# Kernel optimization log

Hardware: AMD Instinct MI355X
Metric: run time of the kernel (lower is better)

## Reference

```python
import jax, jax.numpy as jnp
import numpy as np

B, N, C, CP, H, NK = 1, 2048, 128, 16, 8, 128
D = C // H
W_HALF = NK // 2
EPS = 1e-5
NEG = -1e9


def _ln(x, scale=None, bias=None):
    m = jnp.mean(x, axis=-1, keepdims=True)
    v = jnp.var(x, axis=-1, keepdims=True)
    y = (x - m) * jax.lax.rsqrt(v + EPS)
    if scale is not None:
        y = y * scale
    if bias is not None:
        y = y + bias
    return y


def _ada_ln(a, s, s_scale, gate_w, gate_b, skip_w):
    # AF3 AdaLN: a <- sigmoid(Lin(LN(s))) * LN(a) + LinNoBias(LN(s))
    sn = _ln(s, s_scale)
    return jax.nn.sigmoid(sn @ gate_w + gate_b) * _ln(a) + sn @ skip_w


def setup_inputs() -> dict:
    key = jax.random.key(0)
    ks = jax.random.split(key, 24)

    def w(k, shape, fan_in):
        return jax.random.normal(k, shape, jnp.float32) / np.float32(np.sqrt(fan_in))

    return {
        'atom_single_repr': jax.random.normal(ks[0], (B, N, C), jnp.float32),
        'atom_single_proj': jax.random.normal(ks[1], (B, N, C), jnp.float32),
        'atom_pair_repr': jax.random.normal(ks[2], (B, N, N, CP), jnp.float32),
        'mask': jnp.ones((B, N), jnp.float32),
        # AttentionPairBias AdaLN
        'adaln_s_scale': jnp.ones((C,), jnp.float32),
        'adaln_gate_w': w(ks[3], (C, C), C),
        'adaln_gate_b': jnp.zeros((C,), jnp.float32),
        'adaln_skip_w': w(ks[4], (C, C), C),
        # attention projections
        'wq': w(ks[5], (C, H * D), C),
        'wk': w(ks[6], (C, H * D), C),
        'wv': w(ks[7], (C, H * D), C),
        'wg': w(ks[8], (C, H * D), C),
        'bg': jnp.ones((H * D,), jnp.float32),
        'wo': w(ks[9], (H * D, C), H * D),
        'bo': jnp.zeros((C,), jnp.float32),
        # pair bias
        'pair_ln_scale': jnp.ones((CP,), jnp.float32),
        'pair_ln_bias': jnp.zeros((CP,), jnp.float32),
        'w_pair': w(ks[10], (CP, H), CP),
        # adaLN-zero output gate (bias init -2)
        'out_gate_w': w(ks[11], (C, C), C),
        'out_gate_b': jnp.full((C,), -2.0, jnp.float32),
        # ConditionedTransitionBlock AdaLN
        't_s_scale': jnp.ones((C,), jnp.float32),
        't_gate_w': w(ks[12], (C, C), C),
        't_gate_b': jnp.zeros((C,), jnp.float32),
        't_skip_w': w(ks[13], (C, C), C),
        # SwiGLU transition, expansion n=2
        't_swish_w': w(ks[14], (C, 2 * C), C),
        't_hidden_w': w(ks[15], (C, 2 * C), C),
        't_out_w': w(ks[16], (2 * C, C), 2 * C),
        't_out_gate_w': w(ks[17], (C, C), C),
        't_out_gate_b': jnp.full((C,), -2.0, jnp.float32),
    }


def reference(atom_single_repr, atom_single_proj, atom_pair_repr, mask,
              adaln_s_scale, adaln_gate_w, adaln_gate_b, adaln_skip_w,
              wq, wk, wv, wg, bg, wo, bo,
              pair_ln_scale, pair_ln_bias, w_pair,
              out_gate_w, out_gate_b,
              t_s_scale, t_gate_w, t_gate_b, t_skip_w,
              t_swish_w, t_hidden_w, t_out_w, t_out_gate_w, t_out_gate_b):
    b, n, _ = atom_single_repr.shape
    # --- AttentionPairBias ---
    a = _ada_ln(atom_single_repr, atom_single_proj,
                adaln_s_scale, adaln_gate_w, adaln_gate_b, adaln_skip_w)
    # pair bias [b,h,n,n]
    bias = jnp.transpose(_ln(atom_pair_repr, pair_ln_scale, pair_ln_bias) @ w_pair, (0, 3, 1, 2))
    idx = jnp.arange(n)
    diff = idx[None, :] - idx[:, None]  # j - i
    win = (diff >= -W_HALF) & (diff <= W_HALF)  # sliding window (left,right)=(64,64)
    bias = bias + jnp.where(win, 0.0, NEG)[None, None]
    bias = bias + (1e9 * (mask - 1.0))[:, None, None, :]
    q = (a @ wq).reshape(b, n, H, D) * (D ** -0.5)
    k = (a @ wk).reshape(b, n, H, D)
    v = (a @ wv).reshape(b, n, H, D)
    attn = jax.nn.softmax(jnp.einsum('bqhd,bkhd->bhqk', q, k) + bias, axis=-1)
    o = jnp.einsum('bhqk,bkhd->bqhd', attn, v)
    g = jax.nn.sigmoid(a @ wg + bg).reshape(b, n, H, D)  # per-head output gating
    attn_out = (o * g).reshape(b, n, H * D) @ wo + bo
    attn_out = jax.nn.sigmoid(atom_single_proj @ out_gate_w + out_gate_b) * attn_out
    # --- ConditionedTransitionBlock ---
    t = _ada_ln(atom_single_repr, atom_single_proj,
                t_s_scale, t_gate_w, t_gate_b, t_skip_w)
    hid = jax.nn.silu(t @ t_swish_w) * (t @ t_hidden_w)  # SwiGLU
    trans = jax.nn.sigmoid(atom_single_proj @ t_out_gate_w + t_out_gate_b) * (hid @ t_out_w)
    return attn_out + trans
```

## Files before the change

### kernel.cpp

```cpp
#include <hip/hip_runtime.h>

#define NN 2048
#define CC 128
#define CPC 16
#define HH 8
#define DD 16
#define WHALF 64

__device__ __forceinline__ float sigf(float x){ return 1.0f/(1.0f+__expf(-x)); }

__global__ __launch_bounds__(256) void ln_both(const float* __restrict__ a,
                                               const float* __restrict__ s,
                                               float* __restrict__ ln_a,
                                               float* __restrict__ ln_s){
  const float* x = blockIdx.y ? s : a;
  float* ln = blockIdx.y ? ln_s : ln_a;
  int row = blockIdx.x*4 + (threadIdx.x>>6);
  int lane = threadIdx.x & 63;
  size_t base = (size_t)row*CC;
  float2 v = *(const float2*)(x + base + 2*lane);
  float ssum = v.x+v.y, sq = v.x*v.x+v.y*v.y;
  #pragma unroll
  for (int m=32;m;m>>=1){ ssum += __shfl_xor(ssum,m); sq += __shfl_xor(sq,m); }
  float mean = ssum*(1.0f/CC);
  float var  = sq*(1.0f/CC)-mean*mean;
  float inv  = rsqrtf(var+1e-5f);
  float2 o; o.x=(v.x-mean)*inv; o.y=(v.y-mean)*inv;
  *(float2*)(ln + base + 2*lane) = o;
}

template<int K, int RPT, int NM>
__device__ __forceinline__ void gemm_core(const float* __restrict__ Arows,
                                          const float* __restrict__ scale,
                                          const float* __restrict__ W0,
                                          const float* __restrict__ W1,
                                          int ldw, int colBase,
                                          float acc[NM][RPT][4], float* As){
  const int t = threadIdx.x;
  constexpr int ROWS = RPT*8;
  const int nv = ROWS*K/4;
  for (int i=t;i<nv;i+=256){
    float4 v = ((const float4*)Arows)[i];
    if (scale){
      int kk = (i*4)&(K-1);
      v.x*=scale[kk]; v.y*=scale[kk+1]; v.z*=scale[kk+2]; v.w*=scale[kk+3];
    }
    ((float4*)As)[i]=v;
  }
  __syncthreads();
  const int tr = t>>5;
  const int col = colBase + (t&31)*4;
  #pragma unroll
  for(int m=0;m<NM;m++)
    #pragma unroll
    for(int r=0;r<RPT;r++){ acc[m][r][0]=0;acc[m][r][1]=0;acc[m][r][2]=0;acc[m][r][3]=0; }
  #pragma unroll 4
  for (int k=0;k<K;k++){
    float a[RPT];
    #pragma unroll
    for (int r=0;r<RPT;r++) a[r]=As[(tr*RPT+r)*K+k];
    {
      float4 w = *(const float4*)(W0 + (size_t)k*ldw + col);
      #pragma unroll
      for (int r=0;r<RPT;r++){acc[0][r][0]+=a[r]*w.x;acc[0][r][1]+=a[r]*w.y;acc[0][r][2]+=a[r]*w.z;acc[0][r][3]+=a[r]*w.w;}
    }
    if constexpr (NM>1){
      float4 w = *(const float4*)(W1 + (size_t)k*ldw + col);
      #pragma unroll
      for (int r=0;r<RPT;r++){acc[1][r][0]+=a[r]*w.x;acc[1][r][1]+=a[r]*w.y;acc[1][r][2]+=a[r]*w.z;acc[1][r][3]+=a[r]*w.w;}
    }
  }
}

__global__ __launch_bounds__(256) void k_gates(const float* __restrict__ s,
    const float* __restrict__ W0, const float* __restrict__ b0,
    const float* __restrict__ W1, const float* __restrict__ b1,
    float* __restrict__ sgog, float* __restrict__ sgtg){
  __shared__ float As[8*128];
  float acc[2][1][4];
  const int row0 = blockIdx.x*8;
  gemm_core<128,1,2>(s + (size_t)row0*CC, nullptr, W0, W1, 128, 0, acc, As);
  const int col = (threadIdx.x&31)*4;
  const int row = row0 + (threadIdx.x>>5);
  float4 v0 = *(const float4*)(b0+col);
  float4 v1 = *(const float4*)(b1+col);
  float4 o0, o1;
  o0.x=sigf(acc[0][0][0]+v0.x); o0.y=sigf(acc[0][0][1]+v0.y); o0.z=sigf(acc[0][0][2]+v0.z); o0.w=sigf(acc[0][0][3]+v0.w);
  o1.x=sigf(acc[1][0][0]+v1.x); o1.y=sigf(acc[1][0][1]+v1.y); o1.z=sigf(acc[1][0][2]+v1.z); o1.w=sigf(acc[1][0][3]+v1.w);
  *(float4*)(sgog + (size_t)row*CC + col) = o0;
  *(float4*)(sgtg + (size_t)row*CC + col) = o1;
}

__global__ __launch_bounds__(256) void k_adaln(const float* __restrict__ ln_s,
    const float* __restrict__ sscale,
    const float* __restrict__ gate_w, const float* __restrict__ gate_b,
    const float* __restrict__ skip_w, const float* __restrict__ ln_a,
    float* __restrict__ outp){
  __shared__ float As[8*128];
  float acc[2][1][4];
  const int row0 = blockIdx.x*8;
  gemm_core<128,1,2>(ln_s + (size_t)row0*CC, sscale, gate_w, skip_w, 128, 0, acc, As);
  const int col = (threadIdx.x&31)*4;
  const int row = row0 + (threadIdx.x>>5);
  float4 gb = *(const float4*)(gate_b+col);
  float4 la = *(const float4*)(ln_a + (size_t)row*CC + col);
  float4 o;
  o.x = sigf(acc[0][0][0]+gb.x)*la.x + acc[1][0][0];
  o.y = sigf(acc[0][0][1]+gb.y)*la.y + acc[1][0][1];
  o.z = sigf(acc[0][0][2]+gb.z)*la.z + acc[1][0][2];
  o.w = sigf(acc[0][0][3]+gb.w)*la.w + acc[1][0][3];
  *(float4*)(outp + (size_t)row*CC + col) = o;
}

__global__ __launch_bounds__(256) void k_qkvg(const float* __restrict__ A,
    const float* __restrict__ wq, const float* __restrict__ wk,
    const float* __restrict__ wv, const float* __restrict__ wg,
    const float* __restrict__ bg,
    float* __restrict__ qb, float* __restrict__ kb,
    float* __restrict__ vb, float* __restrict__ gg){
  __shared__ float As[16*128];
  float acc[2][2][4];
  const int row0 = blockIdx.x*16;
  const int y = blockIdx.y;
  const float* W0 = y ? wv : wq;
  const float* W1 = y ? wg : wk;
  gemm_core<128,2,2>(A + (size_t)row0*CC, nullptr, W0, W1, 128, 0, acc, As);
  const int col = (threadIdx.x&31)*4;
  float* O0 = y ? vb : qb;
  float* O1 = y ? gg : kb;
  float4 b1 = {0,0,0,0};
  if (y) b1 = *(const float4*)(bg+col);
  #pragma unroll
  for (int r=0;r<2;r++){
    const int row = row0 + (threadIdx.x>>5)*2 + r;
    float4 o0 = {acc[0][r][0],acc[0][r][1],acc[0][r][2],acc[0][r][3]};
    float4 o1 = {acc[1][r][0]+b1.x,acc[1][r][1]+b1.y,acc[1][r][2]+b1.z,acc[1][r][3]+b1.w};
    *(float4*)(O0 + (size_t)row*CC + col) = o0;
    *(float4*)(O1 + (size_t)row*CC + col) = o1;
  }
}

__global__ __launch_bounds__(256) void k_wo(const float* __restrict__ A,
    const float* __restrict__ W, const float* __restrict__ b,
    float* __restrict__ outp){
  __shared__ float As[8*128];
  float acc[1][1][4];
  const int row0 = blockIdx.x*8;
  gemm_core<128,1,1>(A + (size_t)row0*CC, nullptr, W, nullptr, 128, 0, acc, As);
  const int col = (threadIdx.x&31)*4;
  const int row = row0 + (threadIdx.x>>5);
  float4 bb = *(const float4*)(b+col);
  float4 o = {acc[0][0][0]+bb.x, acc[0][0][1]+bb.y, acc[0][0][2]+bb.z, acc[0][0][3]+bb.w};
  *(float4*)(outp + (size_t)row*CC + col) = o;
}

__global__ __launch_bounds__(256) void k_swiglu(const float* __restrict__ A,
    const float* __restrict__ sw_w, const float* __restrict__ hd_w,
    float* __restrict__ hid){
  __shared__ float As[8*128];
  float acc[2][1][4];
  const int row0 = blockIdx.x*8;
  const int cb = blockIdx.y*128;
  gemm_core<128,1,2>(A + (size_t)row0*CC, nullptr, sw_w, hd_w, 256, cb, acc, As);
  const int col = cb + (threadIdx.x&31)*4;
  const int row = row0 + (threadIdx.x>>5);
  float4 o;
  o.x = acc[0][0][0]*sigf(acc[0][0][0])*acc[1][0][0];
  o.y = acc[0][0][1]*sigf(acc[0][0][1])*acc[1][0][1];
  o.z = acc[0][0][2]*sigf(acc[0][0][2])*acc[1][0][2];
  o.w = acc[0][0][3]*sigf(acc[0][0][3])*acc[1][0][3];
  *(float4*)(hid + (size_t)row*256 + col) = o;
}

__global__ __launch_bounds__(256) void k_tout(const float* __restrict__ hid,
    const float* __restrict__ W,
    const float* __restrict__ sgog, const float* __restrict__ aout,
    const float* __restrict__ sgtg, float* __restrict__ outp){
  __shared__ float As[8*256];
  float acc[1][1][4];
  const int row0 = blockIdx.x*8;
  gemm_core<256,1,1>(hid + (size_t)row0*256, nullptr, W, nullptr, 128, 0, acc, As);
  const int col = (threadIdx.x&31)*4;
  const int row = row0 + (threadIdx.x>>5);
  float4 g0 = *(const float4*)(sgog + (size_t)row*CC + col);
  float4 ao = *(const float4*)(aout + (size_t)row*CC + col);
  float4 g1 = *(const float4*)(sgtg + (size_t)row*CC + col);
  float4 o;
  o.x = g0.x*ao.x + g1.x*acc[0][0][0];
  o.y = g0.y*ao.y + g1.y*acc[0][0][1];
  o.z = g0.z*ao.z + g1.z*acc[0][0][2];
  o.w = g0.w*ao.w + g1.w*acc[0][0][3];
  *(float4*)(outp + (size_t)row*CC + col) = o;
}

__global__ __launch_bounds__(256) void attn_win(const float* __restrict__ q,
    const float* __restrict__ k, const float* __restrict__ v,
    const float* __restrict__ g, const float* __restrict__ pair,
    const float* __restrict__ pls, const float* __restrict__ plb,
    const float* __restrict__ w_pair, const float* __restrict__ mask,
    float* __restrict__ o_out) {
  __shared__ __align__(16) float qs[CC];
  __shared__ float sc[HH][132];
  __shared__ float wp[CPC][HH];
  __shared__ float plss[CPC], plbs[CPC];
  __shared__ float inv_sum[HH];
  const int i = blockIdx.x;
  const int t = threadIdx.x;
  if (t < CC) qs[t] = q[(size_t)i*CC + t] * 0.25f;
  if (t < CPC*HH) wp[t>>3][t&7] = w_pair[t];
  if (t >= 128 && t < 128+CPC){ plss[t-128]=pls[t-128]; plbs[t-128]=plb[t-128]; }
  __syncthreads();
  const int jlo = (i-WHALF > 0) ? i-WHALF : 0;
  const int jhi = (i+WHALF < NN-1) ? i+WHALF : NN-1;
  const int nj = jhi - jlo + 1;
  if (t < nj){
    const int j = jlo + t;
    float pv[CPC]; float s=0.f, sq=0.f;
    const float4* pp4 = (const float4*)(pair + ((size_t)i*NN + j)*CPC);
    #pragma unroll
    for (int c4=0;c4<CPC/4;c4++){
      float4 x4 = pp4[c4];
      pv[c4*4]=x4.x; pv[c4*4+1]=x4.y; pv[c4*4+2]=x4.z; pv[c4*4+3]=x4.w;
      s += x4.x+x4.y+x4.z+x4.w;
      sq += x4.x*x4.x+x4.y*x4.y+x4.z*x4.z+x4.w*x4.w;
    }
    float mean = s*(1.0f/CPC);
    float var  = sq*(1.0f/CPC)-mean*mean;
    float inv  = rsqrtf(var+1e-5f);
    #pragma unroll
    for (int c=0;c<CPC;c++) pv[c] = (pv[c]-mean)*inv*plss[c] + plbs[c];
    float mterm = 1e9f*(mask[j]-1.0f);
    const float4* kr4 = (const float4*)(k + (size_t)j*CC);
    const float4* qs4 = (const float4*)qs;
    #pragma unroll
    for (int h=0;h<HH;h++){
      float bias = 0.f;
      #pragma unroll
      for (int c=0;c<CPC;c++) bias += pv[c]*wp[c][h];
      float d = 0.f;
      #pragma unroll
      for (int w=0;w<4;w++){
        float4 kk = kr4[h*4+w];
        float4 qq = qs4[h*4+w];
        d += kk.x*qq.x + kk.y*qq.y + kk.z*qq.z + kk.w*qq.w;
      }
      sc[h][t] = d + bias + mterm;
    }
  }
  __syncthreads();
  {
    const int h = t >> 5;
    const int l = t & 31;
    float m = -1e30f;
    for (int jj=l; jj<nj; jj+=32) m = fmaxf(m, sc[h][jj]);
    #pragma unroll
    for (int mm=16;mm;mm>>=1) m = fmaxf(m, __shfl_xor(m,mm));
    float ss = 0.f;
    for (int jj=l; jj<nj; jj+=32){ float e=__expf(sc[h][jj]-m); sc[h][jj]=e; ss+=e; }
    #pragma unroll
    for (int mm=16;mm;mm>>=1) ss += __shfl_xor(ss,mm);
    if (l==0) inv_sum[h] = 1.0f/ss;
  }
  __syncthreads();
  if (t < CC){
    const int h = t >> 4;
    float acc = 0.f;
    for (int jj=0; jj<nj; jj++)
      acc += sc[h][jj] * v[(size_t)(jlo+jj)*CC + t];
    float gate = sigf(g[(size_t)i*CC + t]);
    o_out[(size_t)i*CC + t] = acc * inv_sum[h] * gate;
  }
}

extern "C" void kernel_launch(void* const* d_in, const int* in_sizes, int n_in,
                              void* d_out, int out_size, void* d_ws, size_t ws_size,
                              hipStream_t stream) {
  const float* a_in = (const float*)d_in[0];
  const float* s_in = (const float*)d_in[1];
  const float* pair = (const float*)d_in[2];
  const float* mask = (const float*)d_in[3];
  const float* adaln_s_scale = (const float*)d_in[4];
  const float* adaln_gate_w  = (const float*)d_in[5];
  const float* adaln_gate_b  = (const float*)d_in[6];
  const float* adaln_skip_w  = (const float*)d_in[7];
  const float* wq = (const float*)d_in[8];
  const float* wk = (const float*)d_in[9];
  const float* wv = (const float*)d_in[10];
  const float* wg = (const float*)d_in[11];
  const float* bg = (const float*)d_in[12];
  const float* wo = (const float*)d_in[13];
  const float* bo = (const float*)d_in[14];
  const float* pls = (const float*)d_in[15];
  const float* plb = (const float*)d_in[16];
  const float* w_pair = (const float*)d_in[17];
  const float* out_gate_w = (const float*)d_in[18];
  const float* out_gate_b = (const float*)d_in[19];
  const float* t_s_scale  = (const float*)d_in[20];
  const float* t_gate_w   = (const float*)d_in[21];
  const float* t_gate_b   = (const float*)d_in[22];
  const float* t_skip_w   = (const float*)d_in[23];
  const float* t_swish_w  = (const float*)d_in[24];
  const float* t_hidden_w = (const float*)d_in[25];
  const float* t_out_w    = (const float*)d_in[26];
  const float* t_out_gate_w = (const float*)d_in[27];
  const float* t_out_gate_b = (const float*)d_in[28];

  float* ws = (float*)d_ws;
  const size_t U = (size_t)NN*CC;
  float* ln_a  = ws + 0*U;
  float* ln_s  = ws + 1*U;
  float* sg_og = ws + 2*U;
  float* sg_tg = ws + 3*U;
  float* a_att = ws + 4*U;
  float* tcond = ws + 5*U;
  float* qb    = ws + 6*U;
  float* kb    = ws + 7*U;
  float* vb    = ws + 8*U;
  float* gg    = ws + 9*U;
  float* o_gat = ws + 10*U;
  float* aout  = ws + 11*U;
  float* hid   = ws + 12*U;

  dim3 blk(256);
  ln_both<<<dim3(NN/4,2), blk, 0, stream>>>(a_in, s_in, ln_a, ln_s);
  k_gates<<<NN/8, blk, 0, stream>>>(s_in, out_gate_w, out_gate_b, t_out_gate_w, t_out_gate_b, sg_og, sg_tg);
  k_adaln<<<NN/8, blk, 0, stream>>>(ln_s, adaln_s_scale, adaln_gate_w, adaln_gate_b, adaln_skip_w, ln_a, a_att);
  k_adaln<<<NN/8, blk, 0, stream>>>(ln_s, t_s_scale, t_gate_w, t_gate_b, t_skip_w, ln_a, tcond);
  k_qkvg<<<dim3(NN/16,2), blk, 0, stream>>>(a_att, wq, wk, wv, wg, bg, qb, kb, vb, gg);
  attn_win<<<NN, blk, 0, stream>>>(qb, kb, vb, gg, pair, pls, plb, w_pair, mask, o_gat);
  k_wo<<<NN/8, blk, 0, stream>>>(o_gat, wo, bo, aout);
  k_swiglu<<<dim3(NN/8,2), blk, 0, stream>>>(tcond, t_swish_w, t_hidden_w, hid);
  k_tout<<<NN/8, blk, 0, stream>>>(hid, t_out_w, sg_og, aout, sg_tg, (float*)d_out);
}
```

Baseline: 535.5 us.

## Fuse layernorms, gates, AdaLN and output GEMMs; use all threads in attention

Merges the layernorm, gate and both AdaLN kernels into one three-way kernel that computes layernorms in registers. QKVG is split four ways, and the Wo and transition-out GEMMs are fused into one final kernel. Together this cuts the launch count from nine to five and avoids workspace round-trips for ln_a, ln_s and aout. Inside windowed attention, all 256 threads now compute scores, with each half covering four heads, and the PV reduction is split across two thread halves. The q scaling and gate sigmoid move into the projection epilogue, and the extra reductions add small shared-memory syncs.

```diff
diff --git a/kernel.cpp b/kernel.cpp
--- a/kernel.cpp
+++ b/kernel.cpp
@@ -9,188 +9,149 @@
 
 __device__ __forceinline__ float sigf(float x){ return 1.0f/(1.0f+__expf(-x)); }
 
-__global__ __launch_bounds__(256) void ln_both(const float* __restrict__ a,
-                                               const float* __restrict__ s,
-                                               float* __restrict__ ln_a,
-                                               float* __restrict__ ln_s){
-  const float* x = blockIdx.y ? s : a;
-  float* ln = blockIdx.y ? ln_s : ln_a;
-  int row = blockIdx.x*4 + (threadIdx.x>>6);
-  int lane = threadIdx.x & 63;
-  size_t base = (size_t)row*CC;
-  float2 v = *(const float2*)(x + base + 2*lane);
-  float ssum = v.x+v.y, sq = v.x*v.x+v.y*v.y;
-  #pragma unroll
-  for (int m=32;m;m>>=1){ ssum += __shfl_xor(ssum,m); sq += __shfl_xor(sq,m); }
-  float mean = ssum*(1.0f/CC);
-  float var  = sq*(1.0f/CC)-mean*mean;
-  float inv  = rsqrtf(var+1e-5f);
-  float2 o; o.x=(v.x-mean)*inv; o.y=(v.y-mean)*inv;
-  *(float2*)(ln + base + 2*lane) = o;
-}
-
-template<int K, int RPT, int NM>
-__device__ __forceinline__ void gemm_core(const float* __restrict__ Arows,
-                                          const float* __restrict__ scale,
-                                          const float* __restrict__ W0,
-                                          const float* __restrict__ W1,
-                                          int ldw, int colBase,
-                                          float acc[NM][RPT][4], float* As){
-  const int t = threadIdx.x;
-  constexpr int ROWS = RPT*8;
-  const int nv = ROWS*K/4;
-  for (int i=t;i<nv;i+=256){
-    float4 v = ((const float4*)Arows)[i];
-    if (scale){
-      int kk = (i*4)&(K-1);
-      v.x*=scale[kk]; v.y*=scale[kk+1]; v.z*=scale[kk+2]; v.w*=scale[kk+3];
+__global__ __launch_bounds__(256) void k_pre(
+    const float* __restrict__ a_in, const float* __restrict__ s_in,
+    const float* __restrict__ ada_sc, const float* __restrict__ ada_gw,
+    const float* __restrict__ ada_gb, const float* __restrict__ ada_sw,
+    const float* __restrict__ t_sc, const float* __restrict__ t_gw,
+    const float* __restrict__ t_gb, const float* __restrict__ t_sw,
+    const float* __restrict__ og_w, const float* __restrict__ og_b,
+    const float* __restrict__ tg_w, const float* __restrict__ tg_b,
+    float* __restrict__ sg_og, float* __restrict__ sg_tg,
+    float* __restrict__ a_att, float* __restrict__ tcond)
+{
+  __shared__ float As[8*CC];
+  __shared__ float Ls[8*CC];
+  const int y = blockIdx.y;
+  const int row0 = blockIdx.x*8;
+  const int t = threadIdx.x;
+  const int tr = t>>5, col = (t&31)*4;
+  {
+    float4 v = *(const float4*)(s_in + (size_t)(row0+tr)*CC + col);
+    if (y==0){
+      *(float4*)(As + t*4) = v;
+    } else {
+      float s1 = v.x+v.y+v.z+v.w;
+      float s2 = v.x*v.x+v.y*v.y+v.z*v.z+v.w*v.w;
+      #pragma unroll
+      for (int m=16;m;m>>=1){ s1+=__shfl_xor(s1,m); s2+=__shfl_xor(s2,m); }
+      float mean=s1*(1.0f/CC), var=s2*(1.0f/CC)-mean*mean, inv=rsqrtf(var+1e-5f);
+      const float* sc = (y==1)? ada_sc : t_sc;
+      float4 scv = *(const float4*)(sc+col);
+      float4 o; o.x=(v.x-mean)*inv*scv.x; o.y=(v.y-mean)*inv*scv.y;
+                o.z=(v.z-mean)*inv*scv.z; o.w=(v.w-mean)*inv*scv.w;
+      *(float4*)(As + t*4) = o;
+      float4 av = *(const float4*)(a_in + (size_t)(row0+tr)*CC + col);
+      float a1 = av.x+av.y+av.z+av.w;
+      float a2 = av.x*av.x+av.y*av.y+av.z*av.z+av.w*av.w;
+      #pragma unroll
+      for (int m=16;m;m>>=1){ a1+=__shfl_xor(a1,m); a2+=__shfl_xor(a2,m); }
+      float am=a1*(1.0f/CC), avr=a2*(1.0f/CC)-am*am, ai=rsqrtf(avr+1e-5f);
+      float4 la; la.x=(av.x-am)*ai; la.y=(av.y-am)*ai;
+                 la.z=(av.z-am)*ai; la.w=(av.w-am)*ai;
+      *(float4*)(Ls + t*4) = la;
     }
-    ((float4*)As)[i]=v;
-  }
-  __syncthreads();
-  const int tr = t>>5;
-  const int col = colBase + (t&31)*4;
-  #pragma unroll
-  for(int m=0;m<NM;m++)
-    #pragma unroll
-    for(int r=0;r<RPT;r++){ acc[m][r][0]=0;acc[m][r][1]=0;acc[m][r][2]=0;acc[m][r][3]=0; }
-  #pragma unroll 4
-  for (int k=0;k<K;k++){
-    float a[RPT];
-    #pragma unroll
-    for (int r=0;r<RPT;r++) a[r]=As[(tr*RPT+r)*K+k];
-    {
-      float4 w = *(const float4*)(W0 + (size_t)k*ldw + col);
-      #pragma unroll
-      for (int r=0;r<RPT;r++){acc[0][r][0]+=a[r]*w.x;acc[0][r][1]+=a[r]*w.y;acc[0][r][2]+=a[r]*w.z;acc[0][r][3]+=a[r]*w.w;}
-    }
-    if constexpr (NM>1){
-      float4 w = *(const float4*)(W1 + (size_t)k*ldw + col);
-      #pragma unroll
-      for (int r=0;r<RPT;r++){acc[1][r][0]+=a[r]*w.x;acc[1][r][1]+=a[r]*w.y;acc[1][r][2]+=a[r]*w.z;acc[1][r][3]+=a[r]*w.w;}
-    }
-  }
-}
-
-__global__ __launch_bounds__(256) void k_gates(const float* __restrict__ s,
-    const float* __restrict__ W0, const float* __restrict__ b0,
-    const float* __restrict__ W1, const float* __restrict__ b1,
-    float* __restrict__ sgog, float* __restrict__ sgtg){
-  __shared__ float As[8*128];
-  float acc[2][1][4];
-  const int row0 = blockIdx.x*8;
-  gemm_core<128,1,2>(s + (size_t)row0*CC, nullptr, W0, W1, 128, 0, acc, As);
-  const int col = (threadIdx.x&31)*4;
-  const int row = row0 + (threadIdx.x>>5);
-  float4 v0 = *(const float4*)(b0+col);
-  float4 v1 = *(const float4*)(b1+col);
-  float4 o0, o1;
-  o0.x=sigf(acc[0][0][0]+v0.x); o0.y=sigf(acc[0][0][1]+v0.y); o0.z=sigf(acc[0][0][2]+v0.z); o0.w=sigf(acc[0][0][3]+v0.w);
-  o1.x=sigf(acc[1][0][0]+v1.x); o1.y=sigf(acc[1][0][1]+v1.y); o1.z=sigf(acc[1][0][2]+v1.z); o1.w=sigf(acc[1][0][3]+v1.w);
-  *(float4*)(sgog + (size_t)row*CC + col) = o0;
-  *(float4*)(sgtg + (size_t)row*CC + col) = o1;
-}
-
-__global__ __launch_bounds__(256) void k_adaln(const float* __restrict__ ln_s,
-    const float* __restrict__ sscale,
-    const float* __restrict__ gate_w, const float* __restrict__ gate_b,
-    const float* __restrict__ skip_w, const float* __restrict__ ln_a,
-    float* __restrict__ outp){
-  __shared__ float As[8*128];
-  float acc[2][1][4];
-  const int row0 = blockIdx.x*8;
-  gemm_core<128,1,2>(ln_s + (size_t)row0*CC, sscale, gate_w, skip_w, 128, 0, acc, As);
-  const int col = (threadIdx.x&31)*4;
-  const int row = row0 + (threadIdx.x>>5);
-  float4 gb = *(const float4*)(gate_b+col);
-  float4 la = *(const float4*)(ln_a + (size_t)row*CC + col);
-  float4 o;
-  o.x = sigf(acc[0][0][0]+gb.x)*la.x + acc[1][0][0];
-  o.y = sigf(acc[0][0][1]+gb.y)*la.y + acc[1][0][1];
-  o.z = sigf(acc[0][0][2]+gb.z)*la.z + acc[1][0][2];
-  o.w = sigf(acc[0][0][3]+gb.w)*la.w + acc[1][0][3];
-  *(float4*)(outp + (size_t)row*CC + col) = o;
-}
-
-__global__ __launch_bounds__(256) void k_qkvg(const float* __restrict__ A,
+  }
+  __syncthreads();
+  const float* W0 = (y==0)? og_w : ((y==1)? ada_gw : t_gw);
+  const float* W1 = (y==0)? tg_w : ((y==1)? ada_sw : t_sw);
+  float acc0[4]={0,0,0,0}, acc1[4]={0,0,0,0};
+  #pragma unroll 4
+  for (int k=0;k<CC;k++){
+    float a = As[tr*CC+k];
+    float4 w0 = *(const float4*)(W0 + (size_t)k*CC + col);
+    float4 w1 = *(const float4*)(W1 + (size_t)k*CC + col);
+    acc0[0]+=a*w0.x; acc0[1]+=a*w0.y; acc0[2]+=a*w0.z; acc0[3]+=a*w0.w;
+    acc1[0]+=a*w1.x; acc1[1]+=a*w1.y; acc1[2]+=a*w1.z; acc1[3]+=a*w1.w;
+  }
+  const size_t off = (size_t)(row0+tr)*CC + col;
+  if (y==0){
+    float4 b0 = *(const float4*)(og_b+col);
+    float4 b1 = *(const float4*)(tg_b+col);
+    float4 o0 = {sigf(acc0[0]+b0.x),sigf(acc0[1]+b0.y),sigf(acc0[2]+b0.z),sigf(acc0[3]+b0.w)};
+    float4 o1 = {sigf(acc1[0]+b1.x),sigf(acc1[1]+b1.y),sigf(acc1[2]+b1.z),sigf(acc1[3]+b1.w)};
+    *(float4*)(sg_og+off)=o0; *(float4*)(sg_tg+off)=o1;
+  } else {
+    const float* gbp = (y==1)? ada_gb : t_gb;
+    float4 gb = *(const float4*)(gbp+col);
+    float4 la = *(const float4*)(Ls + t*4);
+    float4 o;
+    o.x = sigf(acc0[0]+gb.x)*la.x + acc1[0];
+    o.y = sigf(acc0[1]+gb.y)*la.y + acc1[1];
+    o.z = sigf(acc0[2]+gb.z)*la.z + acc1[2];
+    o.w = sigf(acc0[3]+gb.w)*la.w + acc1[3];
+    float* dst = (y==1)? a_att : tcond;
+    *(float4*)(dst+off)=o;
+  }
+}
+
+__global__ __launch_bounds__(256) void k_qkvg4(const float* __restrict__ A,
     const float* __restrict__ wq, const float* __restrict__ wk,
     const float* __restrict__ wv, const float* __restrict__ wg,
     const float* __restrict__ bg,
     float* __restrict__ qb, float* __restrict__ kb,
-    float* __restrict__ vb, float* __restrict__ gg){
-  __shared__ float As[16*128];
-  float acc[2][2][4];
-  const int row0 = blockIdx.x*16;
+    float* __restrict__ vb, float* __restrict__ gg)
+{
+  __shared__ float As[8*CC];
   const int y = blockIdx.y;
-  const float* W0 = y ? wv : wq;
-  const float* W1 = y ? wg : wk;
-  gemm_core<128,2,2>(A + (size_t)row0*CC, nullptr, W0, W1, 128, 0, acc, As);
-  const int col = (threadIdx.x&31)*4;
-  float* O0 = y ? vb : qb;
-  float* O1 = y ? gg : kb;
-  float4 b1 = {0,0,0,0};
-  if (y) b1 = *(const float4*)(bg+col);
-  #pragma unroll
-  for (int r=0;r<2;r++){
-    const int row = row0 + (threadIdx.x>>5)*2 + r;
-    float4 o0 = {acc[0][r][0],acc[0][r][1],acc[0][r][2],acc[0][r][3]};
-    float4 o1 = {acc[1][r][0]+b1.x,acc[1][r][1]+b1.y,acc[1][r][2]+b1.z,acc[1][r][3]+b1.w};
-    *(float4*)(O0 + (size_t)row*CC + col) = o0;
-    *(float4*)(O1 + (size_t)row*CC + col) = o1;
-  }
-}
-
-__global__ __launch_bounds__(256) void k_wo(const float* __restrict__ A,
-    const float* __restrict__ W, const float* __restrict__ b,
-    float* __restrict__ outp){
-  __shared__ float As[8*128];
-  float acc[1][1][4];
   const int row0 = blockIdx.x*8;
-  gemm_core<128,1,1>(A + (size_t)row0*CC, nullptr, W, nullptr, 128, 0, acc, As);
-  const int col = (threadIdx.x&31)*4;
-  const int row = row0 + (threadIdx.x>>5);
-  float4 bb = *(const float4*)(b+col);
-  float4 o = {acc[0][0][0]+bb.x, acc[0][0][1]+bb.y, acc[0][0][2]+bb.z, acc[0][0][3]+bb.w};
-  *(float4*)(outp + (size_t)row*CC + col) = o;
+  const int t = threadIdx.x;
+  const int tr = t>>5, col=(t&31)*4;
+  *(float4*)(As + t*4) = *(const float4*)(A + (size_t)(row0+tr)*CC + col);
+  __syncthreads();
+  const float* W = (y==0)?wq:((y==1)?wk:((y==2)?wv:wg));
+  float acc[4]={0,0,0,0};
+  #pragma unroll 4
+  for (int k=0;k<CC;k++){
+    float a = As[tr*CC+k];
+    float4 w = *(const float4*)(W + (size_t)k*CC + col);
+    acc[0]+=a*w.x; acc[1]+=a*w.y; acc[2]+=a*w.z; acc[3]+=a*w.w;
+  }
+  const size_t off = (size_t)(row0+tr)*CC + col;
+  float4 o;
+  if (y==0){
+    o.x=acc[0]*0.25f; o.y=acc[1]*0.25f; o.z=acc[2]*0.25f; o.w=acc[3]*0.25f;
+    *(float4*)(qb+off)=o;
+  } else if (y==1){
+    o.x=acc[0]; o.y=acc[1]; o.z=acc[2]; o.w=acc[3];
+    *(float4*)(kb+off)=o;
+  } else if (y==2){
+    o.x=acc[0]; o.y=acc[1]; o.z=acc[2]; o.w=acc[3];
+    *(float4*)(vb+off)=o;
+  } else {
+    float4 b=*(const float4*)(bg+col);
+    o.x=sigf(acc[0]+b.x); o.y=sigf(acc[1]+b.y); o.z=sigf(acc[2]+b.z); o.w=sigf(acc[3]+b.w);
+    *(float4*)(gg+off)=o;
+  }
 }
 
 __global__ __launch_bounds__(256) void k_swiglu(const float* __restrict__ A,
     const float* __restrict__ sw_w, const float* __restrict__ hd_w,
-    float* __restrict__ hid){
-  __shared__ float As[8*128];
-  float acc[2][1][4];
+    float* __restrict__ hid)
+{
+  __shared__ float As[8*CC];
   const int row0 = blockIdx.x*8;
   const int cb = blockIdx.y*128;
-  gemm_core<128,1,2>(A + (size_t)row0*CC, nullptr, sw_w, hd_w, 256, cb, acc, As);
-  const int col = cb + (threadIdx.x&31)*4;
-  const int row = row0 + (threadIdx.x>>5);
+  const int t = threadIdx.x;
+  const int tr=t>>5, c32=(t&31)*4;
+  *(float4*)(As+t*4) = *(const float4*)(A + (size_t)(row0+tr)*CC + c32);
+  __syncthreads();
+  const int col = cb + c32;
+  float a0[4]={0,0,0,0}, a1[4]={0,0,0,0};
+  #pragma unroll 4
+  for (int k=0;k<CC;k++){
+    float a=As[tr*CC+k];
+    float4 w0=*(const float4*)(sw_w + (size_t)k*256 + col);
+    float4 w1=*(const float4*)(hd_w + (size_t)k*256 + col);
+    a0[0]+=a*w0.x; a0[1]+=a*w0.y; a0[2]+=a*w0.z; a0[3]+=a*w0.w;
+    a1[0]+=a*w1.x; a1[1]+=a*w1.y; a1[2]+=a*w1.z; a1[3]+=a*w1.w;
+  }
   float4 o;
-  o.x = acc[0][0][0]*sigf(acc[0][0][0])*acc[1][0][0];
-  o.y = acc[0][0][1]*sigf(acc[0][0][1])*acc[1][0][1];
-  o.z = acc[0][0][2]*sigf(acc[0][0][2])*acc[1][0][2];
-  o.w = acc[0][0][3]*sigf(acc[0][0][3])*acc[1][0][3];
-  *(float4*)(hid + (size_t)row*256 + col) = o;
-}
-
-__global__ __launch_bounds__(256) void k_tout(const float* __restrict__ hid,
-    const float* __restrict__ W,
-    const float* __restrict__ sgog, const float* __restrict__ aout,
-    const float* __restrict__ sgtg, float* __restrict__ outp){
-  __shared__ float As[8*256];
-  float acc[1][1][4];
-  const int row0 = blockIdx.x*8;
-  gemm_core<256,1,1>(hid + (size_t)row0*256, nullptr, W, nullptr, 128, 0, acc, As);
-  const int col = (threadIdx.x&31)*4;
-  const int row = row0 + (threadIdx.x>>5);
-  float4 g0 = *(const float4*)(sgog + (size_t)row*CC + col);
-  float4 ao = *(const float4*)(aout + (size_t)row*CC + col);
-  float4 g1 = *(const float4*)(sgtg + (size_t)row*CC + col);
-  float4 o;
-  o.x = g0.x*ao.x + g1.x*acc[0][0][0];
-  o.y = g0.y*ao.y + g1.y*acc[0][0][1];
-  o.z = g0.z*ao.z + g1.z*acc[0][0][2];
-  o.w = g0.w*ao.w + g1.w*acc[0][0][3];
-  *(float4*)(outp + (size_t)row*CC + col) = o;
+  o.x=a0[0]*sigf(a0[0])*a1[0];
+  o.y=a0[1]*sigf(a0[1])*a1[1];
+  o.z=a0[2]*sigf(a0[2])*a1[2];
+  o.w=a0[3]*sigf(a0[3])*a1[3];
+  *(float4*)(hid + (size_t)(row0+tr)*256 + col) = o;
 }
 
 __global__ __launch_bounds__(256) void attn_win(const float* __restrict__ q,
@@ -204,17 +165,19 @@
   __shared__ float wp[CPC][HH];
   __shared__ float plss[CPC], plbs[CPC];
   __shared__ float inv_sum[HH];
+  __shared__ float pa[256];
   const int i = blockIdx.x;
   const int t = threadIdx.x;
-  if (t < CC) qs[t] = q[(size_t)i*CC + t] * 0.25f;
-  if (t < CPC*HH) wp[t>>3][t&7] = w_pair[t];
-  if (t >= 128 && t < 128+CPC){ plss[t-128]=pls[t-128]; plbs[t-128]=plb[t-128]; }
+  if (t < CC) qs[t] = q[(size_t)i*CC + t];
+  if (t < CPC){ plss[t]=pls[t]; plbs[t]=plb[t]; }
+  if (t >= CC){ int u=t-CC; wp[u>>3][u&7]=w_pair[u]; }
   __syncthreads();
   const int jlo = (i-WHALF > 0) ? i-WHALF : 0;
   const int jhi = (i+WHALF < NN-1) ? i+WHALF : NN-1;
   const int nj = jhi - jlo + 1;
-  if (t < nj){
-    const int j = jlo + t;
+  const int tt = t & 127, grp = t>>7;
+  for (int jj = tt; jj < nj; jj += 128){
+    const int j = jlo + jj;
     float pv[CPC]; float s=0.f, sq=0.f;
     const float4* pp4 = (const float4*)(pair + ((size_t)i*NN + j)*CPC);
     #pragma unroll
@@ -233,7 +196,8 @@
     const float4* kr4 = (const float4*)(k + (size_t)j*CC);
     const float4* qs4 = (const float4*)qs;
     #pragma unroll
-    for (int h=0;h<HH;h++){
+    for (int hh=0;hh<4;hh++){
+      const int h = grp*4 + hh;
       float bias = 0.f;
       #pragma unroll
       for (int c=0;c<CPC;c++) bias += pv[c]*wp[c][h];
@@ -244,7 +208,7 @@
         float4 qq = qs4[h*4+w];
         d += kk.x*qq.x + kk.y*qq.y + kk.z*qq.z + kk.w*qq.w;
       }
-      sc[h][t] = d + bias + mterm;
+      sc[h][jj] = d + bias + mterm;
     }
   }
   __syncthreads();
@@ -262,14 +226,62 @@
     if (l==0) inv_sum[h] = 1.0f/ss;
   }
   __syncthreads();
-  if (t < CC){
-    const int h = t >> 4;
+  {
+    const int c = t & 127, half = t>>7;
+    const int h = c >> 4;
     float acc = 0.f;
-    for (int jj=0; jj<nj; jj++)
-      acc += sc[h][jj] * v[(size_t)(jlo+jj)*CC + t];
-    float gate = sigf(g[(size_t)i*CC + t]);
-    o_out[(size_t)i*CC + t] = acc * inv_sum[h] * gate;
-  }
+    for (int jj=half; jj<nj; jj+=2)
+      acc += sc[h][jj] * v[(size_t)(jlo+jj)*CC + c];
+    pa[t] = acc;
+    __syncthreads();
+    if (t < CC){
+      float o = (pa[t] + pa[t+CC]) * inv_sum[h] * g[(size_t)i*CC + t];
+      o_out[(size_t)i*CC + t] = o;
+    }
+  }
+}
+
+__global__ __launch_bounds__(256) void k_final(const float* __restrict__ og,
+    const float* __restrict__ wo, const float* __restrict__ bo,
+    const float* __restrict__ hid, const float* __restrict__ tw,
+    const float* __restrict__ sgog, const float* __restrict__ sgtg,
+    float* __restrict__ outp)
+{
+  __shared__ float As[8*CC];
+  __shared__ float Hs[8*256];
+  const int row0 = blockIdx.x*8;
+  const int t = threadIdx.x;
+  const int tr=t>>5, col=(t&31)*4;
+  *(float4*)(As+t*4) = *(const float4*)(og + (size_t)(row0+tr)*CC + col);
+  {
+    const float4* src=(const float4*)(hid + (size_t)row0*256);
+    float4* dst=(float4*)Hs;
+    dst[t]=src[t]; dst[t+256]=src[t+256];
+  }
+  __syncthreads();
+  float acc0[4]={0,0,0,0}, acc1[4]={0,0,0,0};
+  #pragma unroll 4
+  for (int k=0;k<256;k++){
+    float a=Hs[tr*256+k];
+    float4 w=*(const float4*)(tw + (size_t)k*CC + col);
+    acc0[0]+=a*w.x; acc0[1]+=a*w.y; acc0[2]+=a*w.z; acc0[3]+=a*w.w;
+  }
+  #pragma unroll 4
+  for (int k=0;k<CC;k++){
+    float a=As[tr*CC+k];
+    float4 w=*(const float4*)(wo + (size_t)k*CC + col);
+    acc1[0]+=a*w.x; acc1[1]+=a*w.y; acc1[2]+=a*w.z; acc1[3]+=a*w.w;
+  }
+  const size_t off=(size_t)(row0+tr)*CC+col;
+  float4 bb=*(const float4*)(bo+col);
+  float4 g0=*(const float4*)(sgog+off);
+  float4 g1=*(const float4*)(sgtg+off);
+  float4 o;
+  o.x=g0.x*(acc1[0]+bb.x)+g1.x*acc0[0];
+  o.y=g0.y*(acc1[1]+bb.y)+g1.y*acc0[1];
+  o.z=g0.z*(acc1[2]+bb.z)+g1.z*acc0[2];
+  o.w=g0.w*(acc1[3]+bb.w)+g1.w*acc0[3];
+  *(float4*)(outp+off)=o;
 }
 
 extern "C" void kernel_launch(void* const* d_in, const int* in_sizes, int n_in,
@@ -307,28 +319,25 @@
 
   float* ws = (float*)d_ws;
   const size_t U = (size_t)NN*CC;
-  float* ln_a  = ws + 0*U;
-  float* ln_s  = ws + 1*U;
-  float* sg_og = ws + 2*U;
-  float* sg_tg = ws + 3*U;
-  float* a_att = ws + 4*U;
-  float* tcond = ws + 5*U;
-  float* qb    = ws + 6*U;
-  float* kb    = ws + 7*U;
-  float* vb    = ws + 8*U;
-  float* gg    = ws + 9*U;
-  float* o_gat = ws + 10*U;
-  float* aout  = ws + 11*U;
-  float* hid   = ws + 12*U;
+  float* sg_og = ws + 0*U;
+  float* sg_tg = ws + 1*U;
+  float* a_att = ws + 2*U;
+  float* tcond = ws + 3*U;
+  float* qb    = ws + 4*U;
+  float* kb    = ws + 5*U;
+  float* vb    = ws + 6*U;
+  float* gg    = ws + 7*U;
+  float* o_gat = ws + 8*U;
+  float* hid   = ws + 9*U;
 
   dim3 blk(256);
-  ln_both<<<dim3(NN/4,2), blk, 0, stream>>>(a_in, s_in, ln_a, ln_s);
-  k_gates<<<NN/8, blk, 0, stream>>>(s_in, out_gate_w, out_gate_b, t_out_gate_w, t_out_gate_b, sg_og, sg_tg);
-  k_adaln<<<NN/8, blk, 0, stream>>>(ln_s, adaln_s_scale, adaln_gate_w, adaln_gate_b, adaln_skip_w, ln_a, a_att);
-  k_adaln<<<NN/8, blk, 0, stream>>>(ln_s, t_s_scale, t_gate_w, t_gate_b, t_skip_w, ln_a, tcond);
-  k_qkvg<<<dim3(NN/16,2), blk, 0, stream>>>(a_att, wq, wk, wv, wg, bg, qb, kb, vb, gg);
+  k_pre<<<dim3(NN/8,3), blk, 0, stream>>>(a_in, s_in,
+      adaln_s_scale, adaln_gate_w, adaln_gate_b, adaln_skip_w,
+      t_s_scale, t_gate_w, t_gate_b, t_skip_w,
+      out_gate_w, out_gate_b, t_out_gate_w, t_out_gate_b,
+      sg_og, sg_tg, a_att, tcond);
+  k_qkvg4<<<dim3(NN/8,4), blk, 0, stream>>>(a_att, wq, wk, wv, wg, bg, qb, kb, vb, gg);
+  k_swiglu<<<dim3(NN/8,2), blk, 0, stream>>>(tcond, t_swish_w, t_hidden_w, hid);
   attn_win<<<NN, blk, 0, stream>>>(qb, kb, vb, gg, pair, pls, plb, w_pair, mask, o_gat);
-  k_wo<<<NN/8, blk, 0, stream>>>(o_gat, wo, bo, aout);
-  k_swiglu<<<dim3(NN/8,2), blk, 0, stream>>>(tcond, t_swish_w, t_hidden_w, hid);
-  k_tout<<<NN/8, blk, 0, stream>>>(hid, t_out_w, sg_og, aout, sg_tg, (float*)d_out);
-}
+  k_final<<<NN/8, blk, 0, stream>>>(o_gat, wo, bo, hid, t_out_w, sg_og, sg_tg, (float*)d_out);
+}
```

Result: slower. 580.0 us (+8.3%).
